# Performance work log

Measured on AMD Instinct MI355X. Metric: run time of the kernel, lower is better.

Reference implementation:

```python
import jax, jax.numpy as jnp
import numpy as np

H = 8        # heads
DH = 64      # dim_head
IMG = 32     # image_size
KS = 5       # kernel_size (odd)
SCALE = DH ** -0.5


def _unfold(t, ks):
    # t: (b, c, Hp, Wp) already padded. Returns (b, c*ks*ks, Ho*Wo) with
    # channel-major layout (c outermost, then kh, kw) matching torch F.unfold.
    b, c, Hp, Wp = t.shape
    Ho, Wo = Hp - ks + 1, Wp - ks + 1
    pat = jnp.stack([t[:, :, i:i + Ho, j:j + Wo]
                     for i in range(ks) for j in range(ks)], axis=2)  # (b,c,ks*ks,Ho,Wo)
    return pat.reshape(b, c * ks * ks, Ho * Wo)


def setup_inputs() -> dict:
    key = jax.random.key(0)
    k1, k2, k3, k4 = jax.random.split(key, 4)
    b, n, dim, inner = 2, 1152, 512, 512
    x = jax.random.normal(k1, (b, n, dim), jnp.float32)
    w_qkv = jax.random.normal(k2, (dim, inner * 3), jnp.float32) * 0.02
    w_out = jax.random.normal(k3, (inner, dim), jnp.float32) * 0.02
    b_out = jax.random.normal(k4, (dim,), jnp.float32) * 0.02
    return {"x": x, "w_qkv": w_qkv, "w_out": w_out, "b_out": b_out}


def reference(x, w_qkv, w_out, b_out):
    b, n, dim = x.shape
    img_len = IMG * IMG
    text_len = n - img_len
    NEG = -jnp.finfo(x.dtype).max

    qkv = x @ w_qkv                                   # (b, n, 3*inner)
    q, k, v = jnp.split(qkv, 3, axis=-1)

    def to_heads(t):
        return t.reshape(b, n, H, DH).transpose(0, 2, 1, 3).reshape(b * H, n, DH)

    q = to_heads(q) * SCALE
    k = to_heads(k)
    v = to_heads(v)

    # faithful to source: text slice is t[:, img_seq_len:], image is t[:, -img_seq_len:]
    q_text, q_img = q[:, img_len:], q[:, -img_len:]
    k_text, k_img = k[:, img_len:], k[:, -img_len:]
    v_text, v_img = v[:, img_len:], v[:, -img_len:]

    # ---- text branch. NOTE: source uses non-inplace masked_fill, so the
    # causal mask has NO effect -> plain softmax (faithful reproduction).
    dots_text = jnp.einsum('bid,bjd->bij', q_text, k_text)
    attn_text = jax.nn.softmax(dots_text, axis=-1)
    out_text = jnp.einsum('bij,bjd->bid', attn_text, v_text)

    # ---- image branch: local window via unfold
    def to_loc(t):
        g = t.transpose(0, 2, 1).reshape(b * H, DH, IMG, IMG)
        p = KS // 2
        g = jnp.pad(g, ((0, 0), (0, 0), (p, p), (p, p)))
        u = _unfold(g, KS)  # (bh, DH*KS*KS, img_len), channel-major (d outer)
        # faithful to source rearrange 'b (j d) i -> b i j d' (j outermost),
        # which regroups the channel-major unfold output.
        return u.reshape(b * H, KS * KS, DH, img_len).transpose(0, 3, 1, 2)

    k_loc = to_loc(k_img)  # (bh, img_len, KS*KS, DH)
    v_loc = to_loc(v_img)

    dots_txt = jnp.einsum('bid,bjd->bij', q_img, k_text)     # (bh, img_len, text_len)
    dots_loc = jnp.einsum('bid,bijd->bij', q_img, k_loc)     # (bh, img_len, KS*KS)

    # per-query key index mask (padded positions get index img_len -> never masked)
    p = KS // 2
    idx = jnp.arange(img_len, dtype=jnp.float32).reshape(1, 1, IMG, IMG)
    idx = jnp.pad(idx, ((0, 0), (0, 0), (p, p), (p, p)), constant_values=float(img_len))
    kidx = _unfold(idx, KS).transpose(0, 2, 1)               # (1, img_len, KS*KS)
    qidx = jnp.arange(img_len, dtype=jnp.float32).reshape(1, -1, 1)
    mask_loc = qidx <= kidx                                  # faithful: keep q <= k
    dots_loc = jnp.where(mask_loc, dots_loc, NEG)

    dots_img = jnp.concatenate([dots_txt, dots_loc], axis=-1)
    attn_img = jax.nn.softmax(dots_img, axis=-1)
    out_img = (jnp.einsum('bij,bjd->bid', attn_img[..., :text_len], v_text)
               + jnp.einsum('bij,bijd->bid', attn_img[..., text_len:], v_loc))

    out = jnp.concatenate([out_text, out_img], axis=1)       # (bh, n, DH)
    out = out.reshape(b, H, n, DH).transpose(0, 2, 1, 3).reshape(b, n, H * DH)
    return out @ w_out + b_out
```

## Files before the change

### kernel.cpp

```cpp
#include <hip/hip_runtime.h>
#include <hip/hip_bf16.h>
#include <math.h>

#define NTOK 1152
#define DIM 512
#define NQKV 1536
#define DHEAD 64
#define NBH 16
#define TEXTN 128
#define IMGLEN 1024
#define SEG (NBH * NTOK * DHEAD)
#define STF 68
#define TSTATE_F (NBH * IMGLEN * STF)
#define LPAD 40
#define KTSZ (NBH * TEXTN * DHEAD)

typedef __attribute__((ext_vector_type(8))) short bf16x8;
typedef __attribute__((ext_vector_type(8))) ushort u16x8;
typedef __attribute__((ext_vector_type(4))) float f32x4;

__device__ __forceinline__ ushort f2bf(float f) {
    unsigned u = __float_as_uint(f);
    unsigned r = (u + 0x7FFFu + ((u >> 16) & 1u)) >> 16;
    return (ushort)r;
}
__device__ __forceinline__ float bf2f(ushort u) {
    return __uint_as_float(((unsigned)u) << 16);
}

__global__ __launch_bounds__(256) void prep_x_k(const float* __restrict__ X,
                                                ushort* __restrict__ xhi,
                                                ushort* __restrict__ xlo) {
    int i = (blockIdx.x * 256 + threadIdx.x) * 4;
    float4 v = *(const float4*)(X + i);
    ushort4 h, l;
    h.x = f2bf(v.x); l.x = f2bf(v.x - bf2f(h.x));
    h.y = f2bf(v.y); l.y = f2bf(v.y - bf2f(h.y));
    h.z = f2bf(v.z); l.z = f2bf(v.z - bf2f(h.z));
    h.w = f2bf(v.w); l.w = f2bf(v.w - bf2f(h.w));
    *(ushort4*)(xhi + i) = h;
    *(ushort4*)(xlo + i) = l;
}

__global__ __launch_bounds__(256) void prep_wt_k(const float* __restrict__ W,
                                                 ushort* __restrict__ thi,
                                                 ushort* __restrict__ tlo,
                                                 int K, int N) {
    __shared__ float tile[32][33];
    const int bx = blockIdx.x, by = blockIdx.y;
    const int c = threadIdx.x & 31, r8 = threadIdx.x >> 5;
#pragma unroll
    for (int i = 0; i < 4; ++i) {
        int rr = r8 + i * 8;
        tile[rr][c] = W[(size_t)(by * 32 + rr) * N + bx * 32 + c];
    }
    __syncthreads();
#pragma unroll
    for (int i = 0; i < 4; ++i) {
        int rr = r8 + i * 8;
        float v = tile[c][rr];
        size_t o = (size_t)(bx * 32 + rr) * K + by * 32 + c;
        ushort h = f2bf(v);
        thi[o] = h;
        tlo[o] = f2bf(v - bf2f(h));
    }
}

__global__ __launch_bounds__(256) void gemm_qkv_mfma(const ushort* __restrict__ xhi,
                                                     const ushort* __restrict__ xlo,
                                                     const ushort* __restrict__ wthi,
                                                     const ushort* __restrict__ wtlo,
                                                     float* __restrict__ qh,
                                                     float* __restrict__ kh,
                                                     float* __restrict__ vh,
                                                     ushort* __restrict__ qhi,
                                                     ushort* __restrict__ qlo,
                                                     ushort* __restrict__ kthi,
                                                     ushort* __restrict__ ktlo,
                                                     ushort* __restrict__ vthi,
                                                     ushort* __restrict__ vtlo) {
    __shared__ __align__(16) ushort Ah[128 * LPAD], Al[128 * LPAD];
    __shared__ __align__(16) ushort Bh[64 * LPAD], Bl[64 * LPAD];
    __shared__ __align__(16) float Cb[128 * 68];
    const int tid = threadIdx.x;
    const int lane = tid & 63;
    const int w = tid >> 6;
    const int wm = w >> 1, wn = w & 1;
    const int row0 = blockIdx.y * 128;
    const int col0 = blockIdx.x * 64;

    f32x4 acc[4][2];
#pragma unroll
    for (int a = 0; a < 4; ++a)
#pragma unroll
        for (int b = 0; b < 2; ++b) acc[a][b] = (f32x4){0.f, 0.f, 0.f, 0.f};

    const int arow = tid >> 1;
    const int akb = (tid & 1) * 16;
    const int brow = tid >> 2;
    const int bkb = (tid & 3) * 8;
    const int kf = (lane >> 4) * 8;
    const int lr = lane & 15;
    const int lg = lane >> 4;

    for (int k0 = 0; k0 < DIM; k0 += 32) {
        {
            const size_t g = (size_t)(row0 + arow) * DIM + k0 + akb;
            *(bf16x8*)&Ah[arow * LPAD + akb] = *(const bf16x8*)(xhi + g);
            *(bf16x8*)&Ah[arow * LPAD + akb + 8] = *(const bf16x8*)(xhi + g + 8);
            *(bf16x8*)&Al[arow * LPAD + akb] = *(const bf16x8*)(xlo + g);
            *(bf16x8*)&Al[arow * LPAD + akb + 8] = *(const bf16x8*)(xlo + g + 8);
        }
        {
            const size_t g = (size_t)(col0 + brow) * DIM + k0 + bkb;
            *(bf16x8*)&Bh[brow * LPAD + bkb] = *(const bf16x8*)(wthi + g);
            *(bf16x8*)&Bl[brow * LPAD + bkb] = *(const bf16x8*)(wtlo + g);
        }
        __syncthreads();
        bf16x8 ah[4], al[4], bh[2], bl[2];
#pragma unroll
        for (int mi = 0; mi < 4; ++mi) {
            int rr = wm * 64 + mi * 16 + lr;
            ah[mi] = *(const bf16x8*)&Ah[rr * LPAD + kf];
            al[mi] = *(const bf16x8*)&Al[rr * LPAD + kf];
        }
#pragma unroll
        for (int ni = 0; ni < 2; ++ni) {
            int rr = wn * 32 + ni * 16 + lr;
            bh[ni] = *(const bf16x8*)&Bh[rr * LPAD + kf];
            bl[ni] = *(const bf16x8*)&Bl[rr * LPAD + kf];
        }
#pragma unroll
        for (int mi = 0; mi < 4; ++mi)
#pragma unroll
            for (int ni = 0; ni < 2; ++ni) {
                acc[mi][ni] = __builtin_amdgcn_mfma_f32_16x16x32_bf16(ah[mi], bh[ni], acc[mi][ni], 0, 0, 0);
                acc[mi][ni] = __builtin_amdgcn_mfma_f32_16x16x32_bf16(ah[mi], bl[ni], acc[mi][ni], 0, 0, 0);
                acc[mi][ni] = __builtin_amdgcn_mfma_f32_16x16x32_bf16(al[mi], bh[ni], acc[mi][ni], 0, 0, 0);
            }
        __syncthreads();
    }

#pragma unroll
    for (int mi = 0; mi < 4; ++mi)
#pragma unroll
        for (int ni = 0; ni < 2; ++ni)
#pragma unroll
            for (int j = 0; j < 4; ++j) {
                int lrow = wm * 64 + mi * 16 + lg * 4 + j;
                int lcol = wn * 32 + ni * 16 + lr;
                Cb[lrow * 68 + lcol] = acc[mi][ni][j];
            }
    __syncthreads();

    const int which = col0 >> 9;
    const int hh = (col0 & 511) >> 6;
    const float scale = (which == 0) ? 0.125f : 1.f;
    float* dst = (which == 0) ? qh : ((which == 1) ? kh : vh);

    const int orow = tid >> 1;
    const int och = (tid & 1) * 32;
    const int r = row0 + orow;
    const int b_i = r / NTOK, tok = r - b_i * NTOK;
    const int bhi = b_i * 8 + hh;

    float vals[32];
#pragma unroll
    for (int g = 0; g < 8; ++g) {
        float4 v = *(const float4*)&Cb[orow * 68 + och + g * 4];
        vals[g * 4] = v.x * scale; vals[g * 4 + 1] = v.y * scale;
        vals[g * 4 + 2] = v.z * scale; vals[g * 4 + 3] = v.w * scale;
    }
    {
        float* dp = dst + ((size_t)bhi * NTOK + tok) * DHEAD + och;
#pragma unroll
        for (int g = 0; g < 8; ++g) {
            float4 o;
            o.x = vals[g * 4]; o.y = vals[g * 4 + 1];
            o.z = vals[g * 4 + 2]; o.w = vals[g * 4 + 3];
            *(float4*)(dp + g * 4) = o;
        }
    }
    if (which == 0) {
        size_t qo = ((size_t)bhi * NTOK + tok) * DHEAD + och;
#pragma unroll
        for (int half = 0; half < 2; ++half) {
            u16x8 hh8, ll8;
#pragma unroll
            for (int e = 0; e < 8; ++e) {
                float v = vals[half * 16 + e];
                ushort hv = f2bf(v);
                hh8[e] = hv; ll8[e] = f2bf(v - bf2f(hv));
            }
            *(u16x8*)(qhi + qo + half * 16) = hh8;
            *(u16x8*)(qlo + qo + half * 16) = ll8;
            u16x8 hh9, ll9;
#pragma unroll
            for (int e = 0; e < 8; ++e) {
                float v = vals[half * 16 + 8 + e];
                ushort hv = f2bf(v);
                hh9[e] = hv; ll9[e] = f2bf(v - bf2f(hv));
            }
            *(u16x8*)(qhi + qo + half * 16 + 8) = hh9;
            *(u16x8*)(qlo + qo + half * 16 + 8) = ll9;
        }
    } else if (tok >= IMGLEN) {
        const int tr = tok - IMGLEN;
        if (which == 1) {
            size_t ko = ((size_t)bhi * TEXTN + tr) * DHEAD + och;
#pragma unroll
            for (int half = 0; half < 4; ++half) {
                u16x8 hh8, ll8;
#pragma unroll
                for (int e = 0; e < 8; ++e) {
                    float v = vals[half * 8 + e];
                    ushort hv = f2bf(v);
                    hh8[e] = hv; ll8[e] = f2bf(v - bf2f(hv));
                }
                *(u16x8*)(kthi + ko + half * 8) = hh8;
                *(u16x8*)(ktlo + ko + half * 8) = ll8;
            }
        } else {
#pragma unroll
            for (int e = 0; e < 32; ++e) {
                int d = och + e;
                size_t vo = ((size_t)bhi * DHEAD + d) * TEXTN + tr;
                ushort hv = f2bf(vals[e]);
                vthi[vo] = hv;
                vtlo[vo] = f2bf(vals[e] - bf2f(hv));
            }
        }
    }
}

__global__ __launch_bounds__(256) void attn_text_mfma(const ushort* __restrict__ qhi,
                                                      const ushort* __restrict__ qlo,
                                                      const ushort* __restrict__ kthi,
                                                      const ushort* __restrict__ ktlo,
                                                      const ushort* __restrict__ vthi,
                                                      const ushort* __restrict__ vtlo,
                                                      ushort* __restrict__ ahi,
                                                      ushort* __restrict__ alo,
                                                      float* __restrict__ tstate) {
    __shared__ __align__(16) ushort Phi[4][16][136];
    __shared__ __align__(16) ushort Plo[4][16][136];
    const int bh = blockIdx.x / 18;
    const int tile = blockIdx.x % 18;
    const int wave = threadIdx.x >> 6;
    const int lane = threadIdx.x & 63;
    const int lr = lane & 15, lg = lane >> 4;
    const int kf = lg * 8;
    const int qrow0 = tile * 64 + wave * 16;
    const int tok0 = (tile < 2 ? 1024 + tile * 64 : tile * 64) + wave * 16;

    bf16x8 qah[2], qal[2];
    {
        const size_t qb = ((size_t)bh * NTOK + tok0 + lr) * DHEAD;
#pragma unroll
        for (int c = 0; c < 2; ++c) {
            qah[c] = *(const bf16x8*)(qhi + qb + c * 32 + kf);
            qal[c] = *(const bf16x8*)(qlo + qb + c * 32 + kf);
        }
    }
    f32x4 s[8];
#pragma unroll
    for (int t = 0; t < 8; ++t) s[t] = (f32x4){0.f, 0.f, 0.f, 0.f};
#pragma unroll
    for (int t = 0; t < 8; ++t) {
        const size_t kb = ((size_t)bh * TEXTN + t * 16 + lr) * DHEAD;
#pragma unroll
        for (int c = 0; c < 2; ++c) {
            bf16x8 kbh = *(const bf16x8*)(kthi + kb + c * 32 + kf);
            bf16x8 kbl = *(const bf16x8*)(ktlo + kb + c * 32 + kf);
            s[t] = __builtin_amdgcn_mfma_f32_16x16x32_bf16(qah[c], kbh, s[t], 0, 0, 0);
            s[t] = __builtin_amdgcn_mfma_f32_16x16x32_bf16(qah[c], kbl, s[t], 0, 0, 0);
            s[t] = __builtin_amdgcn_mfma_f32_16x16x32_bf16(qal[c], kbh, s[t], 0, 0, 0);
        }
    }
    float mx[4], sm[4];
#pragma unroll
    for (int r = 0; r < 4; ++r) {
        float v = s[0][r];
#pragma unroll
        for (int t = 1; t < 8; ++t) v = fmaxf(v, s[t][r]);
        mx[r] = v;
    }
#pragma unroll
    for (int msk = 1; msk <= 8; msk <<= 1)
#pragma unroll
        for (int r = 0; r < 4; ++r) mx[r] = fmaxf(mx[r], __shfl_xor(mx[r], msk));
#pragma unroll
    for (int r = 0; r < 4; ++r) sm[r] = 0.f;
#pragma unroll
    for (int t = 0; t < 8; ++t)
#pragma unroll
        for (int r = 0; r < 4; ++r) {
            float p = __expf(s[t][r] - mx[r]);
            s[t][r] = p;
            sm[r] += p;
        }
#pragma unroll
    for (int msk = 1; msk <= 8; msk <<= 1)
#pragma unroll
        for (int r = 0; r < 4; ++r) sm[r] += __shfl_xor(sm[r], msk);
#pragma unroll
    for (int t = 0; t < 8; ++t)
#pragma unroll
        for (int r = 0; r < 4; ++r) {
            float p = s[t][r];
            ushort h = f2bf(p);
            Phi[wave][lg * 4 + r][t * 16 + lr] = h;
            Plo[wave][lg * 4 + r][t * 16 + lr] = f2bf(p - bf2f(h));
        }
    __syncthreads();
    f32x4 o[4];
#pragma unroll
    for (int dt = 0; dt < 4; ++dt) o[dt] = (f32x4){0.f, 0.f, 0.f, 0.f};
#pragma unroll
    for (int c = 0; c < 4; ++c) {
        bf16x8 pah = *(const bf16x8*)&Phi[wave][lr][c * 32 + kf];
        bf16x8 pal = *(const bf16x8*)&Plo[wave][lr][c * 32 + kf];
#pragma unroll
        for (int dt = 0; dt < 4; ++dt) {
            const size_t vb = ((size_t)bh * DHEAD + dt * 16 + lr) * TEXTN + c * 32 + kf;
            bf16x8 vbh = *(const bf16x8*)(vthi + vb);
            bf16x8 vbl = *(const bf16x8*)(vtlo + vb);
            o[dt] = __builtin_amdgcn_mfma_f32_16x16x32_bf16(pah, vbh, o[dt], 0, 0, 0);
            o[dt] = __builtin_amdgcn_mfma_f32_16x16x32_bf16(pah, vbl, o[dt], 0, 0, 0);
            o[dt] = __builtin_amdgcn_mfma_f32_16x16x32_bf16(pal, vbh, o[dt], 0, 0, 0);
        }
    }
    if (tile < 2) {
#pragma unroll
        for (int r = 0; r < 4; ++r) {
            const int row = qrow0 + lg * 4 + r;
            const float inv = 1.f / sm[r];
            const size_t base = ((size_t)bh * NTOK + row) * DHEAD;
#pragma unroll
            for (int dt = 0; dt < 4; ++dt) {
                float v = o[dt][r] * inv;
                ushort h = f2bf(v);
                ahi[base + dt * 16 + lr] = h;
                alo[base + dt * 16 + lr] = f2bf(v - bf2f(h));
            }
        }
    } else {
#pragma unroll
        for (int r = 0; r < 4; ++r) {
            const int imgq = qrow0 - TEXTN + lg * 4 + r;
            float* st = tstate + ((size_t)bh * IMGLEN + imgq) * STF;
#pragma unroll
            for (int dt = 0; dt < 4; ++dt) st[dt * 16 + lr] = o[dt][r];
            if (lr == 0) { st[64] = mx[r]; st[65] = sm[r]; }
        }
    }
}

__global__ __launch_bounds__(64, 1) void attn_img_k(const float* __restrict__ qh,
                                                    const float* __restrict__ kh,
                                                    const float* __restrict__ vh,
                                                    ushort* __restrict__ ahi,
                                                    ushort* __restrict__ alo,
                                                    const float* __restrict__ tstate) {
    __shared__ __align__(16) float Kl[192 * 64];
    __shared__ __align__(16) float Vl[192 * 64];
    __shared__ __align__(16) float Qb[64 * 64];
    const int bh = blockIdx.x >> 4;
    const int qtile = (blockIdx.x & 15) << 6;
    const int yr0 = qtile >> 5;
    const int lane = threadIdx.x;
    const int qq = qtile + lane;
    const int y = qq >> 5, x = qq & 31;
    const int yloc = lane >> 5;
    const float* kimg = kh + (size_t)(bh * NTOK + TEXTN) * DHEAD;
    const float* vimg = vh + (size_t)(bh * NTOK + TEXTN) * DHEAD;
    const float* st = tstate + ((size_t)(bh * IMGLEN + qq)) * STF;

    for (int i = 0; i < 48; ++i) {
        int flat = lane + i * 64;
        int px = flat >> 4, b = flat & 15;
        int gy = yr0 - 2 + (px >> 5), gx = px & 31;
        if (gy >= 0 && gy < 32) {
            size_t off = ((size_t)(gy * 32 + gx)) * DHEAD + b * 4;
            int dsto = px * 64 + ((b ^ (px & 7)) << 2);
            *(float4*)&Kl[dsto] = *(const float4*)(kimg + off);
            *(float4*)&Vl[dsto] = *(const float4*)(vimg + off);
        }
    }
    {
        const float* qbase = qh + ((size_t)(bh * NTOK + TEXTN + qtile)) * DHEAD;
        for (int i = 0; i < 16; ++i) {
            int flat = lane + i * 64;
            int px = flat >> 4, b = flat & 15;
            *(float4*)&Qb[px * 64 + ((b ^ (px & 7)) << 2)] =
                *(const float4*)(qbase + (size_t)px * DHEAD + b * 4);
        }
    }
    __syncthreads();

    float q[64];
#pragma unroll
    for (int b = 0; b < 16; ++b) {
        float4 v = *(const float4*)&Qb[lane * 64 + ((b ^ (lane & 7)) << 2)];
        q[b * 4] = v.x; q[b * 4 + 1] = v.y; q[b * 4 + 2] = v.z; q[b * 4 + 3] = v.w;
    }

    float sd[25];
#pragma unroll
    for (int j = 0; j < 25; ++j) sd[j] = 0.f;
#pragma unroll
    for (int t = 0; t < 25; ++t) {
        const int ny = y + t / 5 - 2;
        const int nx = x + t % 5 - 2;
        if (ny >= 0 && ny < 32 && nx >= 0 && nx < 32) {
            const int px = (yloc + t / 5) * 32 + nx;
            const float* base = Kl + px * 64;
#pragma unroll
            for (int b16 = 0; b16 < 16; ++b16) {
                float4 kv = *(const float4*)(base + ((b16 ^ (px & 7)) << 2));
                float ke[4] = {kv.x, kv.y, kv.z, kv.w};
#pragma unroll
                for (int e = 0; e < 4; ++e) {
                    const int d = b16 * 4 + e;
                    const int id2 = d * 25 + t;
                    sd[id2 >> 6] += q[id2 & 63] * ke[e];
                }
            }
        }
    }

    float m = st[64], l = st[65];
    float mloc = -1e30f;
#pragma unroll
    for (int j = 0; j < 25; ++j) {
        const int my = y + j / 5 - 2;
        const int mx2 = x + j % 5 - 2;
        bool inb = (my >= 0 && my < 32 && mx2 >= 0 && mx2 < 32);
        bool keep = inb ? (qq <= my * 32 + mx2) : true;
        sd[j] = keep ? sd[j] : -1e30f;
        mloc = fmaxf(mloc, sd[j]);
    }
    const float M = fmaxf(m, mloc);
    const float cc = __expf(m - M);
    l *= cc;
#pragma unroll
    for (int j = 0; j < 25; ++j) {
        sd[j] = __expf(sd[j] - M);
        l += sd[j];
    }
    const float inv = 1.f / l;

    float out[64];
#pragma unroll
    for (int g = 0; g < 16; ++g) {
        float4 tv = *(const float4*)(st + g * 4);
        out[g * 4] = cc * tv.x; out[g * 4 + 1] = cc * tv.y;
        out[g * 4 + 2] = cc * tv.z; out[g * 4 + 3] = cc * tv.w;
    }
#pragma unroll
    for (int t = 0; t < 25; ++t) {
        const int ny = y + t / 5 - 2;
        const int nx = x + t % 5 - 2;
        if (ny >= 0 && ny < 32 && nx >= 0 && nx < 32) {
            const int px = (yloc + t / 5) * 32 + nx;
            const float* base = Vl + px * 64;
#pragma unroll
            for (int b16 = 0; b16 < 16; ++b16) {
                float4 vv = *(const float4*)(base + ((b16 ^ (px & 7)) << 2));
                float ve[4] = {vv.x, vv.y, vv.z, vv.w};
#pragma unroll
                for (int e = 0; e < 4; ++e) {
                    const int d = b16 * 4 + e;
                    const int id2 = d * 25 + t;
                    out[id2 & 63] += sd[id2 >> 6] * ve[e];
                }
            }
        }
    }

    const size_t base = ((size_t)(bh * NTOK + TEXTN + qq)) * DHEAD;
#pragma unroll
    for (int g = 0; g < 16; ++g) {
        float v0 = out[g * 4] * inv;
        float v1 = out[g * 4 + 1] * inv;
        float v2 = out[g * 4 + 2] * inv;
        float v3 = out[g * 4 + 3] * inv;
        ushort4 oh, ol;
        oh.x = f2bf(v0); ol.x = f2bf(v0 - bf2f(oh.x));
        oh.y = f2bf(v1); ol.y = f2bf(v1 - bf2f(oh.y));
        oh.z = f2bf(v2); ol.z = f2bf(v2 - bf2f(oh.z));
        oh.w = f2bf(v3); ol.w = f2bf(v3 - bf2f(oh.w));
        *(ushort4*)(ahi + base + g * 4) = oh;
        *(ushort4*)(alo + base + g * 4) = ol;
    }
}

__global__ __launch_bounds__(256) void gemm_out_mfma(const ushort* __restrict__ ahi,
                                                     const ushort* __restrict__ alo,
                                                     const ushort* __restrict__ wthi,
                                                     const ushort* __restrict__ wtlo,
                                                     const float* __restrict__ bias,
                                                     float* __restrict__ Y) {
    __shared__ __align__(16) ushort Ah[128 * LPAD], Al[128 * LPAD];
    __shared__ __align__(16) ushort Bh[64 * LPAD], Bl[64 * LPAD];
    __shared__ __align__(16) float Cb[128 * 68];
    const int tid = threadIdx.x;
    const int lane = tid & 63;
    const int w = tid >> 6;
    const int wm = w >> 1, wn = w & 1;
    const int row0 = blockIdx.y * 128;
    const int col0 = blockIdx.x * 64;

    f32x4 acc[4][2];
#pragma unroll
    for (int a = 0; a < 4; ++a)
#pragma unroll
        for (int b = 0; b < 2; ++b) acc[a][b] = (f32x4){0.f, 0.f, 0.f, 0.f};

    const int arow = tid >> 1;
    const int akb = (tid & 1) * 16;
    const int brow = tid >> 2;
    const int bkb = (tid & 3) * 8;
    const int kf = (lane >> 4) * 8;
    const int lr = lane & 15;
    const int lg = lane >> 4;

    const int ar = row0 + arow;
    const int a_bi = ar / NTOK;
    const int a_tok = ar - a_bi * NTOK;

    for (int k0 = 0; k0 < DIM; k0 += 32) {
        {
            const int kg = k0 + akb;
            const int hh = kg >> 6, d0 = kg & 63;
            const size_t g = ((size_t)(a_bi * 8 + hh) * NTOK + a_tok) * DHEAD + d0;
            *(bf16x8*)&Ah[arow * LPAD + akb] = *(const bf16x8*)(ahi + g);
            *(bf16x8*)&Ah[arow * LPAD + akb + 8] = *(const bf16x8*)(ahi + g + 8);
            *(bf16x8*)&Al[arow * LPAD + akb] = *(const bf16x8*)(alo + g);
            *(bf16x8*)&Al[arow * LPAD + akb + 8] = *(const bf16x8*)(alo + g + 8);
        }
        {
            const size_t g = (size_t)(col0 + brow) * DIM + k0 + bkb;
            *(bf16x8*)&Bh[brow * LPAD + bkb] = *(const bf16x8*)(wthi + g);
            *(bf16x8*)&Bl[brow * LPAD + bkb] = *(const bf16x8*)(wtlo + g);
        }
        __syncthreads();
        bf16x8 ah[4], al[4], bh[2], bl[2];
#pragma unroll
        for (int mi = 0; mi < 4; ++mi) {
            int rr = wm * 64 + mi * 16 + lr;
            ah[mi] = *(const bf16x8*)&Ah[rr * LPAD + kf];
            al[mi] = *(const bf16x8*)&Al[rr * LPAD + kf];
        }
#pragma unroll
        for (int ni = 0; ni < 2; ++ni) {
            int rr = wn * 32 + ni * 16 + lr;
            bh[ni] = *(const bf16x8*)&Bh[rr * LPAD + kf];
            bl[ni] = *(const bf16x8*)&Bl[rr * LPAD + kf];
        }
#pragma unroll
        for (int mi = 0; mi < 4; ++mi)
#pragma unroll
            for (int ni = 0; ni < 2; ++ni) {
                acc[mi][ni] = __builtin_amdgcn_mfma_f32_16x16x32_bf16(ah[mi], bh[ni], acc[mi][ni], 0, 0, 0);
                acc[mi][ni] = __builtin_amdgcn_mfma_f32_16x16x32_bf16(ah[mi], bl[ni], acc[mi][ni], 0, 0, 0);
                acc[mi][ni] = __builtin_amdgcn_mfma_f32_16x16x32_bf16(al[mi], bh[ni], acc[mi][ni], 0, 0, 0);
            }
        __syncthreads();
    }

#pragma unroll
    for (int mi = 0; mi < 4; ++mi)
#pragma unroll
        for (int ni = 0; ni < 2; ++ni)
#pragma unroll
            for (int j = 0; j < 4; ++j) {
                int lrow = wm * 64 + mi * 16 + lg * 4 + j;
                int lcol = wn * 32 + ni * 16 + lr;
                Cb[lrow * 68 + lcol] = acc[mi][ni][j];
            }
    __syncthreads();

    const int orow = tid >> 1;
    const int och = (tid & 1) * 32;
    const int r = row0 + orow;
    float* yp = Y + (size_t)r * DIM + col0 + och;
    const float* bp = bias + col0 + och;
#pragma unroll
    for (int g = 0; g < 8; ++g) {
        float4 v = *(const float4*)&Cb[orow * 68 + och + g * 4];
        float4 b = *(const float4*)(bp + g * 4);
        float4 o;
        o.x = v.x + b.x; o.y = v.y + b.y; o.z = v.z + b.z; o.w = v.w + b.w;
        *(float4*)(yp + g * 4) = o;
    }
}

extern "C" void kernel_launch(void* const* d_in, const int* in_sizes, int n_in,
                              void* d_out, int out_size, void* d_ws, size_t ws_size,
                              hipStream_t stream) {
    const float* x = (const float*)d_in[0];
    const float* w_qkv = (const float*)d_in[1];
    const float* w_out = (const float*)d_in[2];
    const float* b_out = (const float*)d_in[3];
    float* Y = (float*)d_out;
    float* ws = (float*)d_ws;
    float* qh = ws;
    float* kh = ws + (size_t)SEG;
    float* vh = ws + 2 * (size_t)SEG;
    float* tstate = ws + 3 * (size_t)SEG;
    ushort* xhi = (ushort*)(ws + 3 * (size_t)SEG + TSTATE_F);
    ushort* xlo = xhi + (size_t)SEG;
    ushort* ahi = xhi;
    ushort* alo = xlo;
    ushort* wqthi = xlo + (size_t)SEG;
    ushort* wqtlo = wqthi + (size_t)DIM * NQKV;
    ushort* wothi = wqtlo + (size_t)DIM * NQKV;
    ushort* wotlo = wothi + (size_t)DIM * DIM;
    ushort* qhi = wotlo + (size_t)DIM * DIM;
    ushort* qlo = qhi + (size_t)SEG;
    ushort* kthi = qlo + (size_t)SEG;
    ushort* ktlo = kthi + (size_t)KTSZ;
    ushort* vthi = ktlo + (size_t)KTSZ;
    ushort* vtlo = vthi + (size_t)KTSZ;

    hipLaunchKernelGGL(prep_x_k, dim3(SEG / 1024), dim3(256), 0, stream, x, xhi, xlo);
    hipLaunchKernelGGL(prep_wt_k, dim3(NQKV / 32, DIM / 32), dim3(256), 0, stream,
                       w_qkv, wqthi, wqtlo, DIM, NQKV);
    hipLaunchKernelGGL(prep_wt_k, dim3(DIM / 32, DIM / 32), dim3(256), 0, stream,
                       w_out, wothi, wotlo, DIM, DIM);
    hipLaunchKernelGGL(gemm_qkv_mfma, dim3(NQKV / 64, 2304 / 128), dim3(256), 0, stream,
                       xhi, xlo, wqthi, wqtlo, qh, kh, vh,
                       qhi, qlo, kthi, ktlo, vthi, vtlo);
    hipLaunchKernelGGL(attn_text_mfma, dim3(NBH * 18), dim3(256), 0, stream,
                       qhi, qlo, kthi, ktlo, vthi, vtlo, ahi, alo, tstate);
    hipLaunchKernelGGL(attn_img_k, dim3(NBH * 16), dim3(64), 0, stream,
                       qh, kh, vh, ahi, alo, tstate);
    hipLaunchKernelGGL(gemm_out_mfma, dim3(DIM / 64, 2304 / 128), dim3(256), 0, stream,
                       ahi, alo, wothi, wotlo, b_out, Y);
}
```

Measured before the change: 141.8 us.

## Split image local attention across four waves using transposed K/V layout

Adds a kernel that transposes the image K and V to a channel-major layout. The image local-attention kernel moves from one 64-thread wave per block to four waves, each handling 16 of the 64 head dims. Partial scores and partial outputs are reduced through shared memory, and each lane reads K/V straight from global memory with coalesced accesses across neighbouring pixels. This targets the low occupancy and serial per-thread work of the old kernel. The cost is an extra launch, extra global traffic for the transpose, and two more barriers.

```diff
diff --git a/kernel.cpp b/kernel.cpp
--- a/kernel.cpp
+++ b/kernel.cpp
@@ -14,6 +14,7 @@
 #define TSTATE_F (NBH * IMGLEN * STF)
 #define LPAD 40
 #define KTSZ (NBH * TEXTN * DHEAD)
+#define IMGT (NBH * DHEAD * IMGLEN)
 
 typedef __attribute__((ext_vector_type(8))) short bf16x8;
 typedef __attribute__((ext_vector_type(8))) ushort u16x8;
@@ -233,6 +234,48 @@
     }
 }
 
+__global__ __launch_bounds__(256) void trans_kv_k(const float* __restrict__ kh,
+                                                  const float* __restrict__ vh,
+                                                  float* __restrict__ kT,
+                                                  float* __restrict__ vT) {
+    __shared__ float tk[64][65];
+    __shared__ float tv[64][65];
+    const int bh = blockIdx.x >> 4;
+    const int pt0 = (blockIdx.x & 15) * 64;
+    const float* kimg = kh + (size_t)(bh * NTOK + TEXTN) * DHEAD;
+    const float* vimg = vh + (size_t)(bh * NTOK + TEXTN) * DHEAD;
+    {
+        const int p = threadIdx.x >> 2;
+        const int c0 = (threadIdx.x & 3) * 16;
+#pragma unroll
+        for (int i = 0; i < 4; ++i) {
+            float4 kv = *(const float4*)(kimg + (size_t)(pt0 + p) * DHEAD + c0 + i * 4);
+            float4 vv = *(const float4*)(vimg + (size_t)(pt0 + p) * DHEAD + c0 + i * 4);
+            tk[p][c0 + i * 4] = kv.x; tk[p][c0 + i * 4 + 1] = kv.y;
+            tk[p][c0 + i * 4 + 2] = kv.z; tk[p][c0 + i * 4 + 3] = kv.w;
+            tv[p][c0 + i * 4] = vv.x; tv[p][c0 + i * 4 + 1] = vv.y;
+            tv[p][c0 + i * 4 + 2] = vv.z; tv[p][c0 + i * 4 + 3] = vv.w;
+        }
+    }
+    __syncthreads();
+    {
+        const int c = threadIdx.x >> 2;
+        const int p0 = (threadIdx.x & 3) * 16;
+        float* ko = kT + ((size_t)(bh * DHEAD + c)) * IMGLEN + pt0 + p0;
+        float* vo = vT + ((size_t)(bh * DHEAD + c)) * IMGLEN + pt0 + p0;
+#pragma unroll
+        for (int i = 0; i < 4; ++i) {
+            float4 o1, o2;
+            o1.x = tk[p0 + i * 4][c]; o1.y = tk[p0 + i * 4 + 1][c];
+            o1.z = tk[p0 + i * 4 + 2][c]; o1.w = tk[p0 + i * 4 + 3][c];
+            o2.x = tv[p0 + i * 4][c]; o2.y = tv[p0 + i * 4 + 1][c];
+            o2.z = tv[p0 + i * 4 + 2][c]; o2.w = tv[p0 + i * 4 + 3][c];
+            *(float4*)(ko + i * 4) = o1;
+            *(float4*)(vo + i * 4) = o2;
+        }
+    }
+}
+
 __global__ __launch_bounds__(256) void attn_text_mfma(const ushort* __restrict__ qhi,
                                                       const ushort* __restrict__ qlo,
                                                       const ushort* __restrict__ kthi,
@@ -356,142 +399,148 @@
     }
 }
 
-__global__ __launch_bounds__(64, 1) void attn_img_k(const float* __restrict__ qh,
-                                                    const float* __restrict__ kh,
-                                                    const float* __restrict__ vh,
-                                                    ushort* __restrict__ ahi,
-                                                    ushort* __restrict__ alo,
-                                                    const float* __restrict__ tstate) {
-    __shared__ __align__(16) float Kl[192 * 64];
-    __shared__ __align__(16) float Vl[192 * 64];
-    __shared__ __align__(16) float Qb[64 * 64];
-    const int bh = blockIdx.x >> 4;
-    const int qtile = (blockIdx.x & 15) << 6;
-    const int yr0 = qtile >> 5;
-    const int lane = threadIdx.x;
-    const int qq = qtile + lane;
-    const int y = qq >> 5, x = qq & 31;
-    const int yloc = lane >> 5;
-    const float* kimg = kh + (size_t)(bh * NTOK + TEXTN) * DHEAD;
-    const float* vimg = vh + (size_t)(bh * NTOK + TEXTN) * DHEAD;
-    const float* st = tstate + ((size_t)(bh * IMGLEN + qq)) * STF;
-
-    for (int i = 0; i < 48; ++i) {
-        int flat = lane + i * 64;
-        int px = flat >> 4, b = flat & 15;
-        int gy = yr0 - 2 + (px >> 5), gx = px & 31;
-        if (gy >= 0 && gy < 32) {
-            size_t off = ((size_t)(gy * 32 + gx)) * DHEAD + b * 4;
-            int dsto = px * 64 + ((b ^ (px & 7)) << 2);
-            *(float4*)&Kl[dsto] = *(const float4*)(kimg + off);
-            *(float4*)&Vl[dsto] = *(const float4*)(vimg + off);
-        }
-    }
-    {
-        const float* qbase = qh + ((size_t)(bh * NTOK + TEXTN + qtile)) * DHEAD;
-        for (int i = 0; i < 16; ++i) {
-            int flat = lane + i * 64;
-            int px = flat >> 4, b = flat & 15;
-            *(float4*)&Qb[px * 64 + ((b ^ (px & 7)) << 2)] =
-                *(const float4*)(qbase + (size_t)px * DHEAD + b * 4);
-        }
-    }
-    __syncthreads();
-
-    float q[64];
-#pragma unroll
-    for (int b = 0; b < 16; ++b) {
-        float4 v = *(const float4*)&Qb[lane * 64 + ((b ^ (lane & 7)) << 2)];
-        q[b * 4] = v.x; q[b * 4 + 1] = v.y; q[b * 4 + 2] = v.z; q[b * 4 + 3] = v.w;
-    }
-
-    float sd[25];
-#pragma unroll
-    for (int j = 0; j < 25; ++j) sd[j] = 0.f;
+template <int W>
+__device__ inline void loc_dots_t(const float* __restrict__ kTb, int y, int x,
+                                  const float (&q)[64], float (&sd)[25]) {
 #pragma unroll
     for (int t = 0; t < 25; ++t) {
         const int ny = y + t / 5 - 2;
         const int nx = x + t % 5 - 2;
         if (ny >= 0 && ny < 32 && nx >= 0 && nx < 32) {
-            const int px = (yloc + t / 5) * 32 + nx;
-            const float* base = Kl + px * 64;
-#pragma unroll
-            for (int b16 = 0; b16 < 16; ++b16) {
-                float4 kv = *(const float4*)(base + ((b16 ^ (px & 7)) << 2));
-                float ke[4] = {kv.x, kv.y, kv.z, kv.w};
-#pragma unroll
-                for (int e = 0; e < 4; ++e) {
-                    const int d = b16 * 4 + e;
-                    const int id2 = d * 25 + t;
-                    sd[id2 >> 6] += q[id2 & 63] * ke[e];
-                }
-            }
-        }
-    }
-
-    float m = st[64], l = st[65];
-    float mloc = -1e30f;
-#pragma unroll
-    for (int j = 0; j < 25; ++j) {
-        const int my = y + j / 5 - 2;
-        const int mx2 = x + j % 5 - 2;
-        bool inb = (my >= 0 && my < 32 && mx2 >= 0 && mx2 < 32);
-        bool keep = inb ? (qq <= my * 32 + mx2) : true;
-        sd[j] = keep ? sd[j] : -1e30f;
-        mloc = fmaxf(mloc, sd[j]);
-    }
-    const float M = fmaxf(m, mloc);
-    const float cc = __expf(m - M);
-    l *= cc;
-#pragma unroll
-    for (int j = 0; j < 25; ++j) {
-        sd[j] = __expf(sd[j] - M);
-        l += sd[j];
-    }
-    const float inv = 1.f / l;
-
-    float out[64];
-#pragma unroll
-    for (int g = 0; g < 16; ++g) {
-        float4 tv = *(const float4*)(st + g * 4);
-        out[g * 4] = cc * tv.x; out[g * 4 + 1] = cc * tv.y;
-        out[g * 4 + 2] = cc * tv.z; out[g * 4 + 3] = cc * tv.w;
-    }
+            const int px = ny * 32 + nx;
+#pragma unroll
+            for (int g = 0; g < 16; ++g) {
+                const int d = W * 16 + g;
+                float kv = kTb[(size_t)d * IMGLEN + px];
+                const int id2 = d * 25 + t;
+                sd[id2 >> 6] += q[id2 & 63] * kv;
+            }
+        }
+    }
+}
+
+template <int W>
+__device__ inline void loc_pv_t(const float* __restrict__ vTb, int y, int x,
+                                const float (&p)[25], float (&po)[64]) {
 #pragma unroll
     for (int t = 0; t < 25; ++t) {
         const int ny = y + t / 5 - 2;
         const int nx = x + t % 5 - 2;
         if (ny >= 0 && ny < 32 && nx >= 0 && nx < 32) {
-            const int px = (yloc + t / 5) * 32 + nx;
-            const float* base = Vl + px * 64;
-#pragma unroll
-            for (int b16 = 0; b16 < 16; ++b16) {
-                float4 vv = *(const float4*)(base + ((b16 ^ (px & 7)) << 2));
-                float ve[4] = {vv.x, vv.y, vv.z, vv.w};
-#pragma unroll
-                for (int e = 0; e < 4; ++e) {
-                    const int d = b16 * 4 + e;
-                    const int id2 = d * 25 + t;
-                    out[id2 & 63] += sd[id2 >> 6] * ve[e];
-                }
-            }
-        }
-    }
-
-    const size_t base = ((size_t)(bh * NTOK + TEXTN + qq)) * DHEAD;
-#pragma unroll
-    for (int g = 0; g < 16; ++g) {
-        float v0 = out[g * 4] * inv;
-        float v1 = out[g * 4 + 1] * inv;
-        float v2 = out[g * 4 + 2] * inv;
-        float v3 = out[g * 4 + 3] * inv;
-        ushort4 oh, ol;
-        oh.x = f2bf(v0); ol.x = f2bf(v0 - bf2f(oh.x));
-        oh.y = f2bf(v1); ol.y = f2bf(v1 - bf2f(oh.y));
-        oh.z = f2bf(v2); ol.z = f2bf(v2 - bf2f(oh.z));
-        oh.w = f2bf(v3); ol.w = f2bf(v3 - bf2f(oh.w));
-        *(ushort4*)(ahi + base + g * 4) = oh;
-        *(ushort4*)(alo + base + g * 4) = ol;
+            const int px = ny * 32 + nx;
+#pragma unroll
+            for (int g = 0; g < 16; ++g) {
+                const int d = W * 16 + g;
+                float vv = vTb[(size_t)d * IMGLEN + px];
+                const int id2 = d * 25 + t;
+                po[id2 & 63] += p[id2 >> 6] * vv;
+            }
+        }
+    }
+}
+
+__global__ __launch_bounds__(256) void attn_img_k(const float* __restrict__ qh,
+                                                  const float* __restrict__ kT,
+                                                  const float* __restrict__ vT,
+                                                  ushort* __restrict__ ahi,
+                                                  ushort* __restrict__ alo,
+                                                  const float* __restrict__ tstate) {
+    __shared__ float sdb[4][64][27];
+    __shared__ float pob[2][64][68];
+    const int bh = blockIdx.x >> 4;
+    const int qtile = (blockIdx.x & 15) << 6;
+    const int wave = threadIdx.x >> 6;
+    const int lane = threadIdx.x & 63;
+    const int qq = qtile + lane;
+    const int y = qq >> 5, x = qq & 31;
+    const float* kTb = kT + (size_t)bh * DHEAD * IMGLEN;
+    const float* vTb = vT + (size_t)bh * DHEAD * IMGLEN;
+    const float* st = tstate + ((size_t)(bh * IMGLEN + qq)) * STF;
+
+    float sd[25];
+#pragma unroll
+    for (int j = 0; j < 25; ++j) sd[j] = 0.f;
+    {
+        float q[64];
+        const float* qp = qh + ((size_t)(bh * NTOK + TEXTN + qq)) * DHEAD;
+#pragma unroll
+        for (int g = 0; g < 16; ++g) {
+            float4 v4 = *(const float4*)(qp + g * 4);
+            q[g * 4] = v4.x; q[g * 4 + 1] = v4.y; q[g * 4 + 2] = v4.z; q[g * 4 + 3] = v4.w;
+        }
+        if (wave == 0) loc_dots_t<0>(kTb, y, x, q, sd);
+        else if (wave == 1) loc_dots_t<1>(kTb, y, x, q, sd);
+        else if (wave == 2) loc_dots_t<2>(kTb, y, x, q, sd);
+        else loc_dots_t<3>(kTb, y, x, q, sd);
+    }
+#pragma unroll
+    for (int j = 0; j < 25; ++j) sdb[wave][lane][j] = sd[j];
+    __syncthreads();
+
+    float p[25];
+#pragma unroll
+    for (int j = 0; j < 25; ++j)
+        p[j] = (sdb[0][lane][j] + sdb[1][lane][j]) + (sdb[2][lane][j] + sdb[3][lane][j]);
+    float m = st[64], l = st[65];
+    float mloc = -1e30f;
+#pragma unroll
+    for (int j = 0; j < 25; ++j) {
+        const int my = y + j / 5 - 2;
+        const int mx = x + j % 5 - 2;
+        bool inb = (my >= 0 && my < 32 && mx >= 0 && mx < 32);
+        bool keep = inb ? (qq <= my * 32 + mx) : true;
+        p[j] = keep ? p[j] : -1e30f;
+        mloc = fmaxf(mloc, p[j]);
+    }
+    const float M = fmaxf(m, mloc);
+    const float cc = __expf(m - M);
+    l *= cc;
+#pragma unroll
+    for (int j = 0; j < 25; ++j) {
+        p[j] = __expf(p[j] - M);
+        l += p[j];
+    }
+    const float inv = 1.f / l;
+
+    float po[64];
+#pragma unroll
+    for (int o = 0; o < 64; ++o) po[o] = 0.f;
+    if (wave == 0) loc_pv_t<0>(vTb, y, x, p, po);
+    else if (wave == 1) loc_pv_t<1>(vTb, y, x, p, po);
+    else if (wave == 2) loc_pv_t<2>(vTb, y, x, p, po);
+    else loc_pv_t<3>(vTb, y, x, p, po);
+
+    if (wave < 2) {
+#pragma unroll
+        for (int o = 0; o < 64; ++o) pob[wave][lane][o] = po[o];
+    }
+    __syncthreads();
+    if (wave >= 2) {
+#pragma unroll
+        for (int o = 0; o < 64; ++o) pob[wave - 2][lane][o] += po[o];
+    }
+    __syncthreads();
+
+    {
+        const float* stq = st + wave * 16;
+        size_t base = ((size_t)(bh * NTOK + TEXTN + qq)) * DHEAD + wave * 16;
+#pragma unroll
+        for (int g = 0; g < 4; ++g) {
+            float4 tv = *(const float4*)(stq + g * 4);
+            float4 a0 = *(const float4*)&pob[0][lane][wave * 16 + g * 4];
+            float4 a1 = *(const float4*)&pob[1][lane][wave * 16 + g * 4];
+            float v0 = (a0.x + a1.x + cc * tv.x) * inv;
+            float v1 = (a0.y + a1.y + cc * tv.y) * inv;
+            float v2 = (a0.z + a1.z + cc * tv.z) * inv;
+            float v3 = (a0.w + a1.w + cc * tv.w) * inv;
+            ushort4 oh, ol;
+            oh.x = f2bf(v0); ol.x = f2bf(v0 - bf2f(oh.x));
+            oh.y = f2bf(v1); ol.y = f2bf(v1 - bf2f(oh.y));
+            oh.z = f2bf(v2); ol.z = f2bf(v2 - bf2f(oh.z));
+            oh.w = f2bf(v3); ol.w = f2bf(v3 - bf2f(oh.w));
+            *(ushort4*)(ahi + base + g * 4) = oh;
+            *(ushort4*)(alo + base + g * 4) = ol;
+        }
     }
 }
 
@@ -623,6 +672,8 @@
     ushort* ktlo = kthi + (size_t)KTSZ;
     ushort* vthi = ktlo + (size_t)KTSZ;
     ushort* vtlo = vthi + (size_t)KTSZ;
+    float* kimgT = (float*)(vtlo + (size_t)KTSZ);
+    float* vimgT = kimgT + (size_t)IMGT;
 
     hipLaunchKernelGGL(prep_x_k, dim3(SEG / 1024), dim3(256), 0, stream, x, xhi, xlo);
     hipLaunchKernelGGL(prep_wt_k, dim3(NQKV / 32, DIM / 32), dim3(256), 0, stream,
@@ -632,10 +683,12 @@
     hipLaunchKernelGGL(gemm_qkv_mfma, dim3(NQKV / 64, 2304 / 128), dim3(256), 0, stream,
                        xhi, xlo, wqthi, wqtlo, qh, kh, vh,
                        qhi, qlo, kthi, ktlo, vthi, vtlo);
+    hipLaunchKernelGGL(trans_kv_k, dim3(NBH * 16), dim3(256), 0, stream,
+                       kh, vh, kimgT, vimgT);
     hipLaunchKernelGGL(attn_text_mfma, dim3(NBH * 18), dim3(256), 0, stream,
                        qhi, qlo, kthi, ktlo, vthi, vtlo, ahi, alo, tstate);
-    hipLaunchKernelGGL(attn_img_k, dim3(NBH * 16), dim3(64), 0, stream,
-                       qh, kh, vh, ahi, alo, tstate);
+    hipLaunchKernelGGL(attn_img_k, dim3(NBH * 16), dim3(256), 0, stream,
+                       qh, kimgT, vimgT, ahi, alo, tstate);
     hipLaunchKernelGGL(gemm_out_mfma, dim3(DIM / 64, 2304 / 128), dim3(256), 0, stream,
                        ahi, alo, wothi, wotlo, b_out, Y);
 }
```

After: 165.5 us. 16.7% more time.
